# Optimization experiments

Hardware: AMD Instinct MI355X
Metric: run time of the kernel (lower is better)

## Reference

```python
import jax, jax.numpy as jnp
import numpy as np

TEMPLATE_SUBDIVISION = 8
SIGMA = 0.5
NORMALISED = True


def setup_inputs() -> dict:
    key = jax.random.key(0)
    k1, k2, k3 = jax.random.split(key, 3)
    B, N, M_full, D = 2, 32768, 8192, 3
    x = jax.random.normal(k1, (B, N, D), dtype=jnp.float32)
    deformed_verts = jax.random.normal(k2, (B, M_full, D), dtype=jnp.float32)
    mean_shape_verts = jax.random.normal(k3, (B, M_full, D), dtype=jnp.float32)
    deformation_parameters = jnp.zeros((1,), dtype=jnp.float32)  # unused by transform
    return {
        "x": x,
        "deformed_verts": deformed_verts,
        "mean_shape_verts": mean_shape_verts,
        "deformation_parameters": deformation_parameters,
    }


def reference(x, deformed_verts, mean_shape_verts, deformation_parameters):
    # subsample template vertices: [B, M_full, D] -> [B, M, D]
    dv = deformed_verts[:, ::TEMPLATE_SUBDIVISION]
    mv = mean_shape_verts[:, ::TEMPLATE_SUBDIVISION]
    inv_sigma2 = 1.0 / (SIGMA ** 2)
    # broadcast RBF-like kernel: [B, M, N, D]
    kernel_res = jnp.exp(-jnp.abs(x[:, None, :, :] - dv[:, :, None, :]) * inv_sigma2)
    # weighted sum over control vertices M -> [B, N, D]
    out = jnp.sum(mv[:, :, None, :] * kernel_res, axis=1)
    if NORMALISED:
        denominator = jnp.sum(kernel_res, axis=1)
        out = out / denominator
    return out
```

## Files before the change

### kernel.cpp

```cpp
#include <hip/hip_runtime.h>
#include <math.h>

constexpr int B       = 2;
constexpr int N       = 32768;
constexpr int D       = 3;
constexpr int M_FULL  = 8192;
constexpr int SUBDIV  = 8;
constexpr int M       = M_FULL / SUBDIV;
constexpr int K       = 512;
constexpr float LO    = -4.0f;
constexpr float INV_W = 64.0f;
constexpr int BLOCK   = 1024;
constexpr int CHUNKS  = N / BLOCK;
constexpr int GRID    = B * D * CHUNKS;
constexpr float K4    = 5.770780163555852f;

__device__ inline void scan512_pre(float* a) {
    const int lane = threadIdx.x & 63;
    const int base = lane * 8;
    float xv[8], e[8]; float ls = 0.f;
    #pragma unroll
    for (int t = 0; t < 8; ++t) xv[t] = a[base + t];
    #pragma unroll
    for (int t = 0; t < 8; ++t) { e[t] = ls; ls += xv[t]; }
    float inc = ls;
    #pragma unroll
    for (int off = 1; off < 64; off <<= 1) {
        const float tmp = __shfl_up(inc, off, 64);
        if (lane >= off) inc += tmp;
    }
    const float exoff = inc - ls;
    #pragma unroll
    for (int t = 0; t < 8; ++t) a[base + t] = exoff + e[t];
}

__device__ inline void scan512_suf(float* a) {
    const int lane = threadIdx.x & 63;
    const int base = lane * 8;
    float xv[8], e[8]; float ls = 0.f;
    #pragma unroll
    for (int t = 0; t < 8; ++t) xv[t] = a[base + t];
    #pragma unroll
    for (int t = 7; t >= 0; --t) { e[t] = ls; ls += xv[t]; }
    float inc = ls;
    #pragma unroll
    for (int off = 1; off < 64; off <<= 1) {
        const float tmp = __shfl_down(inc, off, 64);
        if (lane + off < 64) inc += tmp;
    }
    const float exoff = inc - ls;
    #pragma unroll
    for (int t = 0; t < 8; ++t) a[base + t] = exoff + e[t] + xv[t];
}

__device__ inline void scan512_i(const int* cntA, int* begA, int* curA) {
    const int lane = threadIdx.x & 63;
    const int base = lane * 8;
    int xv[8], e[8]; int ls = 0;
    #pragma unroll
    for (int t = 0; t < 8; ++t) xv[t] = cntA[base + t];
    #pragma unroll
    for (int t = 0; t < 8; ++t) { e[t] = ls; ls += xv[t]; }
    int inc = ls;
    #pragma unroll
    for (int off = 1; off < 64; off <<= 1) {
        const int tmp = __shfl_up(inc, off, 64);
        if (lane >= off) inc += tmp;
    }
    const int exoff = inc - ls;
    #pragma unroll
    for (int t = 0; t < 8; ++t) {
        begA[base + t] = exoff + e[t];
        curA[base + t] = exoff + e[t];
    }
}

__global__ __launch_bounds__(BLOCK) void deformer_one(
    const float* __restrict__ x,
    const float* __restrict__ dverts,
    const float* __restrict__ mverts,
    float* __restrict__ out)
{
    __shared__ float sV[M], sAp[M], sSp[M], sAm[M], sSm[M];
    __shared__ float gAp[K], gSp[K], gAm[K], gSm[K];
    __shared__ int   cnt[K], beg[K], cur[K];

    const int tid = threadIdx.x;
    const int p = blockIdx.x >> 5;
    const int c = blockIdx.x & 31;
    const int b = p / 3, d = p % 3;

    if (tid < K) {
        cnt[tid] = 0; gAp[tid] = 0.f; gSp[tid] = 0.f; gAm[tid] = 0.f; gSm[tid] = 0.f;
    }
    __syncthreads();

    const int g = (b * M_FULL + tid * SUBDIV) * D + d;
    const float v = dverts[g];
    const float w = mverts[g];
    const float epv = __builtin_amdgcn_exp2f( K4 * v);
    const float emv = __builtin_amdgcn_exp2f(-K4 * v);
    const float ap = w * epv, sp = epv;
    const float am = w * emv, sm = emv;
    int bj = (int)floorf((v - LO) * INV_W);
    bj = bj < 0 ? 0 : (bj > K - 1 ? K - 1 : bj);
    atomicAdd(&cnt[bj], 1);
    atomicAdd(&gAp[bj], ap);
    atomicAdd(&gSp[bj], sp);
    atomicAdd(&gAm[bj], am);
    atomicAdd(&gSm[bj], sm);
    __syncthreads();

    const int wid = tid >> 6;
    if      (wid == 0) scan512_i(cnt, beg, cur);
    else if (wid == 1) scan512_pre(gAp);
    else if (wid == 2) scan512_pre(gSp);
    else if (wid == 3) scan512_suf(gAm);
    else if (wid == 4) scan512_suf(gSm);
    __syncthreads();

    const int pos = atomicAdd(&cur[bj], 1);
    sV[pos] = v; sAp[pos] = ap; sSp[pos] = sp;
    sAm[pos] = am; sSm[pos] = sm;
    __syncthreads();

    const int n = c * BLOCK + tid;
    const int o = (b * N + n) * D + d;
    const float xq = x[o];

    int j = (int)floorf((xq - LO) * INV_W);
    j = j < 0 ? 0 : (j > K - 1 ? K - 1 : j);

    const float en  = __builtin_amdgcn_exp2f(-K4 * xq);
    const float epx = __builtin_amdgcn_exp2f( K4 * xq);

    const float Ap = gAp[j];
    const float Sp = gSp[j];
    const float Am = (j < K - 1) ? gAm[j + 1] : 0.f;
    const float Sm = (j < K - 1) ? gSm[j + 1] : 0.f;

    const int s0 = beg[j], s1 = s0 + cnt[j];
    float rAp = 0.f, rSp = 0.f, rAm = 0.f, rSm = 0.f;
    for (int i = s0; i < s1; ++i) {
        const bool le = (sV[i] <= xq);
        rAp += le ? sAp[i] : 0.f;
        rSp += le ? sSp[i] : 0.f;
        rAm += le ? 0.f : sAm[i];
        rSm += le ? 0.f : sSm[i];
    }
    out[o] = (en * (Ap + rAp) + epx * (Am + rAm)) /
             (en * (Sp + rSp) + epx * (Sm + rSm));
}

extern "C" void kernel_launch(void* const* d_in, const int* in_sizes, int n_in,
                              void* d_out, int out_size, void* d_ws, size_t ws_size,
                              hipStream_t stream) {
    const float* x  = (const float*)d_in[0];
    const float* dv = (const float*)d_in[1];
    const float* mv = (const float*)d_in[2];
    float* out = (float*)d_out;

    deformer_one<<<GRID, BLOCK, 0, stream>>>(x, dv, mv, out);
}
```

Baseline: 67.62 us.

## Split bucket build into a separate kernel and share it across query blocks

```diff
diff --git a/kernel.cpp b/kernel.cpp
--- a/kernel.cpp
+++ b/kernel.cpp
@@ -10,10 +10,15 @@
 constexpr int K       = 512;
 constexpr float LO    = -4.0f;
 constexpr float INV_W = 64.0f;
-constexpr int BLOCK   = 1024;
-constexpr int CHUNKS  = N / BLOCK;
-constexpr int GRID    = B * D * CHUNKS;
 constexpr float K4    = 5.770780163555852f;
+constexpr int NPAIR   = B * D;
+
+constexpr int QBLOCK  = 256;
+constexpr int QCHUNKS = N / QBLOCK;
+constexpr int QGRID   = NPAIR * QCHUNKS;
+
+constexpr int OFF_VW  = 49152;
+constexpr int OFF_BEG = 98304;
 
 __device__ inline void scan512_pre(float* a) {
     const int lane = threadIdx.x & 63;
@@ -75,19 +80,18 @@
     }
 }
 
-__global__ __launch_bounds__(BLOCK) void deformer_one(
-    const float* __restrict__ x,
+__global__ __launch_bounds__(1024) void build_kernel(
     const float* __restrict__ dverts,
     const float* __restrict__ mverts,
-    float* __restrict__ out)
+    float4* __restrict__ aggG,
+    float2* __restrict__ vwG,
+    int*    __restrict__ begG)
 {
-    __shared__ float sV[M], sAp[M], sSp[M], sAm[M], sSm[M];
     __shared__ float gAp[K], gSp[K], gAm[K], gSm[K];
     __shared__ int   cnt[K], beg[K], cur[K];
 
     const int tid = threadIdx.x;
-    const int p = blockIdx.x >> 5;
-    const int c = blockIdx.x & 31;
+    const int p = blockIdx.x;
     const int b = p / 3, d = p % 3;
 
     if (tid < K) {
@@ -100,15 +104,13 @@
     const float w = mverts[g];
     const float epv = __builtin_amdgcn_exp2f( K4 * v);
     const float emv = __builtin_amdgcn_exp2f(-K4 * v);
-    const float ap = w * epv, sp = epv;
-    const float am = w * emv, sm = emv;
     int bj = (int)floorf((v - LO) * INV_W);
     bj = bj < 0 ? 0 : (bj > K - 1 ? K - 1 : bj);
     atomicAdd(&cnt[bj], 1);
-    atomicAdd(&gAp[bj], ap);
-    atomicAdd(&gSp[bj], sp);
-    atomicAdd(&gAm[bj], am);
-    atomicAdd(&gSm[bj], sm);
+    atomicAdd(&gAp[bj], w * epv);
+    atomicAdd(&gSp[bj], epv);
+    atomicAdd(&gAm[bj], w * emv);
+    atomicAdd(&gSm[bj], emv);
     __syncthreads();
 
     const int wid = tid >> 6;
@@ -119,37 +121,69 @@
     else if (wid == 4) scan512_suf(gSm);
     __syncthreads();
 
+    if (tid < K) {
+        const float am = (tid < K - 1) ? gAm[tid + 1] : 0.f;
+        const float sm = (tid < K - 1) ? gSm[tid + 1] : 0.f;
+        aggG[p * K + tid] = make_float4(gAp[tid], gSp[tid], am, sm);
+        begG[p * (K + 1) + tid] = beg[tid];
+        if (tid == 0) begG[p * (K + 1) + K] = M;
+    }
     const int pos = atomicAdd(&cur[bj], 1);
-    sV[pos] = v; sAp[pos] = ap; sSp[pos] = sp;
-    sAm[pos] = am; sSm[pos] = sm;
-    __syncthreads();
-
-    const int n = c * BLOCK + tid;
+    vwG[p * M + pos] = make_float2(v, w);
+}
+
+__global__ __launch_bounds__(QBLOCK) void query_kernel(
+    const float* __restrict__ x,
+    const float4* __restrict__ aggG,
+    const float4* __restrict__ vwG4,
+    const int*    __restrict__ begG,
+    float* __restrict__ out)
+{
+    __shared__ float4 agg[K];
+    __shared__ float2 vw[M];
+    __shared__ int    sbeg[K + 1];
+
+    const int tid = threadIdx.x;
+    const int p = blockIdx.x >> 7;
+    const int c = blockIdx.x & 127;
+    const int b = p / 3, d = p % 3;
+
+    const int n = c * QBLOCK + tid;
     const int o = (b * N + n) * D + d;
     const float xq = x[o];
 
+    agg[tid]        = aggG[p * K + tid];
+    agg[tid + 256]  = aggG[p * K + tid + 256];
+    float4* vwv = (float4*)vw;
+    vwv[tid]        = vwG4[p * (M / 2) + tid];
+    vwv[tid + 256]  = vwG4[p * (M / 2) + tid + 256];
+    sbeg[tid]       = begG[p * (K + 1) + tid];
+    sbeg[tid + 256] = begG[p * (K + 1) + tid + 256];
+    if (tid == 0) sbeg[K] = begG[p * (K + 1) + K];
+    __syncthreads();
+
     int j = (int)floorf((xq - LO) * INV_W);
     j = j < 0 ? 0 : (j > K - 1 ? K - 1 : j);
 
     const float en  = __builtin_amdgcn_exp2f(-K4 * xq);
     const float epx = __builtin_amdgcn_exp2f( K4 * xq);
 
-    const float Ap = gAp[j];
-    const float Sp = gSp[j];
-    const float Am = (j < K - 1) ? gAm[j + 1] : 0.f;
-    const float Sm = (j < K - 1) ? gSm[j + 1] : 0.f;
-
-    const int s0 = beg[j], s1 = s0 + cnt[j];
+    const float4 a = agg[j];
+    const int s0 = sbeg[j], s1 = sbeg[j + 1];
+
     float rAp = 0.f, rSp = 0.f, rAm = 0.f, rSm = 0.f;
     for (int i = s0; i < s1; ++i) {
-        const bool le = (sV[i] <= xq);
-        rAp += le ? sAp[i] : 0.f;
-        rSp += le ? sSp[i] : 0.f;
-        rAm += le ? 0.f : sAm[i];
-        rSm += le ? 0.f : sSm[i];
-    }
-    out[o] = (en * (Ap + rAp) + epx * (Am + rAm)) /
-             (en * (Sp + rSp) + epx * (Sm + rSm));
+        const float2 pv = vw[i];
+        const bool le = (pv.x <= xq);
+        const float t  = __builtin_amdgcn_exp2f(le ? K4 * pv.x : -K4 * pv.x);
+        const float wt = pv.y * t;
+        rAp += le ? wt : 0.f;
+        rSp += le ? t  : 0.f;
+        rAm += le ? 0.f : wt;
+        rSm += le ? 0.f : t;
+    }
+    out[o] = (en * (a.x + rAp) + epx * (a.z + rAm)) /
+             (en * (a.y + rSp) + epx * (a.w + rSm));
 }
 
 extern "C" void kernel_launch(void* const* d_in, const int* in_sizes, int n_in,
@@ -160,5 +194,11 @@
     const float* mv = (const float*)d_in[2];
     float* out = (float*)d_out;
 
-    deformer_one<<<GRID, BLOCK, 0, stream>>>(x, dv, mv, out);
-}
+    char* ws = (char*)d_ws;
+    float4* aggG = (float4*)ws;
+    float2* vwG  = (float2*)(ws + OFF_VW);
+    int*    begG = (int*)(ws + OFF_BEG);
+
+    build_kernel<<<NPAIR, 1024, 0, stream>>>(dv, mv, aggG, vwG, begG);
+    query_kernel<<<QGRID, QBLOCK, 0, stream>>>(x, aggG, (const float4*)vwG, begG, out);
+}
```

After: 69.14 us. 2.3% more time.

## Shrink blocks to 256 threads and compute in-bin terms directly

Applied to the files above, without the earlier changes.

```diff
diff --git a/kernel.cpp b/kernel.cpp
--- a/kernel.cpp
+++ b/kernel.cpp
@@ -10,10 +10,12 @@
 constexpr int K       = 512;
 constexpr float LO    = -4.0f;
 constexpr float INV_W = 64.0f;
-constexpr int BLOCK   = 1024;
+constexpr float K4    = 5.770780163555852f;
+
+constexpr int BLOCK   = 256;
 constexpr int CHUNKS  = N / BLOCK;
 constexpr int GRID    = B * D * CHUNKS;
-constexpr float K4    = 5.770780163555852f;
+constexpr int VPT     = M / BLOCK;
 
 __device__ inline void scan512_pre(float* a) {
     const int lane = threadIdx.x & 63;
@@ -75,58 +77,70 @@
     }
 }
 
-__global__ __launch_bounds__(BLOCK) void deformer_one(
+__global__ __launch_bounds__(BLOCK) void deformer_fused(
     const float* __restrict__ x,
     const float* __restrict__ dverts,
     const float* __restrict__ mverts,
     float* __restrict__ out)
 {
-    __shared__ float sV[M], sAp[M], sSp[M], sAm[M], sSm[M];
-    __shared__ float gAp[K], gSp[K], gAm[K], gSm[K];
-    __shared__ int   cnt[K], beg[K], cur[K];
+    __shared__ float2 vw[M];
+    __shared__ float  gAp[K], gSp[K], gAm[K], gSm[K];
+    __shared__ int    cnt[K], beg[K], cur[K];
 
     const int tid = threadIdx.x;
-    const int p = blockIdx.x >> 5;
-    const int c = blockIdx.x & 31;
+    const int p = blockIdx.x >> 7;
+    const int c = blockIdx.x & 127;
     const int b = p / 3, d = p % 3;
-
-    if (tid < K) {
-        cnt[tid] = 0; gAp[tid] = 0.f; gSp[tid] = 0.f; gAm[tid] = 0.f; gSm[tid] = 0.f;
-    }
-    __syncthreads();
-
-    const int g = (b * M_FULL + tid * SUBDIV) * D + d;
-    const float v = dverts[g];
-    const float w = mverts[g];
-    const float epv = __builtin_amdgcn_exp2f( K4 * v);
-    const float emv = __builtin_amdgcn_exp2f(-K4 * v);
-    const float ap = w * epv, sp = epv;
-    const float am = w * emv, sm = emv;
-    int bj = (int)floorf((v - LO) * INV_W);
-    bj = bj < 0 ? 0 : (bj > K - 1 ? K - 1 : bj);
-    atomicAdd(&cnt[bj], 1);
-    atomicAdd(&gAp[bj], ap);
-    atomicAdd(&gSp[bj], sp);
-    atomicAdd(&gAm[bj], am);
-    atomicAdd(&gSm[bj], sm);
-    __syncthreads();
-
-    const int wid = tid >> 6;
-    if      (wid == 0) scan512_i(cnt, beg, cur);
-    else if (wid == 1) scan512_pre(gAp);
-    else if (wid == 2) scan512_pre(gSp);
-    else if (wid == 3) scan512_suf(gAm);
-    else if (wid == 4) scan512_suf(gSm);
-    __syncthreads();
-
-    const int pos = atomicAdd(&cur[bj], 1);
-    sV[pos] = v; sAp[pos] = ap; sSp[pos] = sp;
-    sAm[pos] = am; sSm[pos] = sm;
-    __syncthreads();
 
     const int n = c * BLOCK + tid;
     const int o = (b * N + n) * D + d;
     const float xq = x[o];
+
+    cnt[tid] = 0;       cnt[tid + 256] = 0;
+    gAp[tid] = 0.f;     gAp[tid + 256] = 0.f;
+    gSp[tid] = 0.f;     gSp[tid + 256] = 0.f;
+    gAm[tid] = 0.f;     gAm[tid + 256] = 0.f;
+    gSm[tid] = 0.f;     gSm[tid + 256] = 0.f;
+    __syncthreads();
+
+    float vv[VPT], wv[VPT];
+    #pragma unroll
+    for (int r = 0; r < VPT; ++r) {
+        const int m = tid + r * BLOCK;
+        const int g = (b * M_FULL + m * SUBDIV) * D + d;
+        vv[r] = dverts[g];
+        wv[r] = mverts[g];
+    }
+    int bjv[VPT];
+    #pragma unroll
+    for (int r = 0; r < VPT; ++r) {
+        const float v = vv[r], w = wv[r];
+        const float epv = __builtin_amdgcn_exp2f( K4 * v);
+        const float emv = __builtin_amdgcn_exp2f(-K4 * v);
+        int bj = (int)floorf((v - LO) * INV_W);
+        bj = bj < 0 ? 0 : (bj > K - 1 ? K - 1 : bj);
+        bjv[r] = bj;
+        atomicAdd(&cnt[bj], 1);
+        atomicAdd(&gAp[bj], w * epv);
+        atomicAdd(&gSp[bj], epv);
+        atomicAdd(&gAm[bj], w * emv);
+        atomicAdd(&gSm[bj], emv);
+    }
+    __syncthreads();
+
+    const int wid = tid >> 6;
+    if      (wid == 0) { scan512_i(cnt, beg, cur); scan512_suf(gSm); }
+    else if (wid == 1) scan512_pre(gAp);
+    else if (wid == 2) scan512_pre(gSp);
+    else if (wid == 3) scan512_suf(gAm);
+    __syncthreads();
+
+    #pragma unroll
+    for (int r = 0; r < VPT; ++r) {
+        const int pos = atomicAdd(&cur[bjv[r]], 1);
+        vw[pos] = make_float2(vv[r], wv[r]);
+    }
+    __syncthreads();
 
     int j = (int)floorf((xq - LO) * INV_W);
     j = j < 0 ? 0 : (j > K - 1 ? K - 1 : j);
@@ -134,22 +148,19 @@
     const float en  = __builtin_amdgcn_exp2f(-K4 * xq);
     const float epx = __builtin_amdgcn_exp2f( K4 * xq);
 
-    const float Ap = gAp[j];
-    const float Sp = gSp[j];
+    const float Ap = gAp[j], Sp = gSp[j];
     const float Am = (j < K - 1) ? gAm[j + 1] : 0.f;
     const float Sm = (j < K - 1) ? gSm[j + 1] : 0.f;
 
-    const int s0 = beg[j], s1 = s0 + cnt[j];
-    float rAp = 0.f, rSp = 0.f, rAm = 0.f, rSm = 0.f;
+    const int s0 = beg[j], s1 = cur[j];
+    float rN = 0.f, rD = 0.f;
     for (int i = s0; i < s1; ++i) {
-        const bool le = (sV[i] <= xq);
-        rAp += le ? sAp[i] : 0.f;
-        rSp += le ? sSp[i] : 0.f;
-        rAm += le ? 0.f : sAm[i];
-        rSm += le ? 0.f : sSm[i];
+        const float2 pv = vw[i];
+        const float e2 = __builtin_amdgcn_exp2f(-K4 * fabsf(xq - pv.x));
+        rN += pv.y * e2;
+        rD += e2;
     }
-    out[o] = (en * (Ap + rAp) + epx * (Am + rAm)) /
-             (en * (Sp + rSp) + epx * (Sm + rSm));
+    out[o] = (en * Ap + epx * Am + rN) / (en * Sp + epx * Sm + rD);
 }
 
 extern "C" void kernel_launch(void* const* d_in, const int* in_sizes, int n_in,
@@ -160,5 +171,5 @@
     const float* mv = (const float*)d_in[2];
     float* out = (float*)d_out;
 
-    deformer_one<<<GRID, BLOCK, 0, stream>>>(x, dv, mv, out);
+    deformer_fused<<<GRID, BLOCK, 0, stream>>>(x, dv, mv, out);
 }
```

Measured after the change: 78.63 us. +16.3%, slower.
